# Kernel optimization log

Measured on AMD Instinct MI355X. Metric: run time of the kernel, lower is better.

The kernel has to match this reference:

```python
import jax, jax.numpy as jnp
import numpy as np

B, S, D = 2, 2048, 768          # batch, n_ctx, d_model
NQK, DQK = 12, 64               # n_qk_heads, d_qk_head
NOV, DOV = 768, 1               # n_ov_heads, d_ov_head
R = NOV // NQK                  # OV heads per QK head
VKV = 4                         # virtual_kv_num
BASE = 10000.0
SCALE = DQK ** 0.5              # cfg.attn_scale default


def _rotary_sin_cos():
    # TransformerLens-style (non-adjacent-pairs): freq repeated as (2 d)
    pos = jnp.arange(S, dtype=jnp.float32)
    freq = BASE ** (jnp.arange(0, DQK, 2, dtype=jnp.float32) / DQK)
    freq = jnp.concatenate([freq, freq])          # [DQK]
    angles = pos[:, None] / freq[None, :]         # [S, DQK]
    return jnp.sin(angles), jnp.cos(angles)


def _apply_rotary(x, sin, cos):
    # x: [b, pos, head, DQK]; rotary_dim == d_qk_head so full rotation
    half = DQK // 2
    rot = jnp.concatenate([-x[..., half:], x[..., :half]], axis=-1)
    return x * cos[None, :, None, :] + rot * sin[None, :, None, :]


def setup_inputs() -> dict:
    key = jax.random.key(0)
    ks = jax.random.split(key, 7)
    std_qk = (2.0 / (D * DQK)) ** 0.5   # kaiming fan_in (d_model*d_head)
    std_ov = (2.0 / (D * DOV)) ** 0.5
    std_o = (2.0 / (DOV * D)) ** 0.5
    sin, cos = _rotary_sin_cos()
    return {
        "resid": jax.random.normal(ks[0], (B, S, D), jnp.float32),
        "W_Q": jax.random.normal(ks[1], (NQK, D, DQK), jnp.float32) * std_qk,
        "W_K": jax.random.normal(ks[2], (NQK, D, DQK), jnp.float32) * std_qk,
        "W_V": jax.random.normal(ks[3], (NOV, D, DOV), jnp.float32) * std_ov,
        "W_O": jax.random.normal(ks[4], (NOV, DOV, D), jnp.float32) * std_o,
        "b_Q": jnp.zeros((NQK, DQK), jnp.float32),
        "b_K": jnp.zeros((NQK, DQK), jnp.float32),
        "b_V": jnp.zeros((NOV, DOV), jnp.float32),
        "virtual_k": jax.random.normal(ks[5], (VKV, NQK, DQK), jnp.float32) * (2.0 / (NQK * DQK)) ** 0.5,
        "virtual_v": jnp.zeros((VKV, NOV, DOV), jnp.float32),  # init zeros, requires_grad=False
        "rotary_sin": sin,
        "rotary_cos": cos,
    }


def reference(resid, W_Q, W_K, W_V, W_O, b_Q, b_K, b_V,
              virtual_k, virtual_v, rotary_sin, rotary_cos):
    # q/k/v projections: per-head low-rank maps + bias  -> [b, s, h, d]
    q = jnp.einsum('bsm,hmd->bshd', resid, W_Q) + b_Q
    k = jnp.einsum('bsm,hmd->bshd', resid, W_K) + b_K
    v = jnp.einsum('bsm,hmd->bshd', resid, W_V) + b_V
    # rotary on q and k
    q = _apply_rotary(q, rotary_sin, rotary_cos)
    k = _apply_rotary(k, rotary_sin, rotary_cos)
    # append virtual KV tokens at the end of the key axis
    k = jnp.concatenate([k, jnp.broadcast_to(virtual_k[None], (B, VKV, NQK, DQK))], axis=1)
    v = jnp.concatenate([v, jnp.broadcast_to(virtual_v[None], (B, VKV, NOV, DOV))], axis=1)
    # full attention scores [b, nqk, S, S+VKV]
    scores = jnp.einsum('bqhd,bkhd->bhqk', q, k) / SCALE
    # causal mask: tril(ones(S, S+VKV), diagonal=VKV) -> key j visible iff j <= i + VKV
    qi = jnp.arange(S)[:, None]
    kj = jnp.arange(S + VKV)[None, :]
    mask = kj <= qi + VKV
    scores = jnp.where(mask[None, None], scores, -jnp.inf)
    pattern = jax.nn.softmax(scores, axis=-1)
    pattern = jnp.where(jnp.isnan(pattern), 0.0, pattern)
    # group OV heads by QK head: v [b, k, NOV, DOV] -> [b, NQK, R, k, DOV]
    v_r = jnp.transpose(v, (0, 2, 1, 3)).reshape(B, NQK, R, S + VKV, DOV)
    z = jnp.einsum('bnqk,bnrkh->bnrqh', pattern, v_r)       # [b, NQK, R, S, DOV]
    z = z.reshape(B, NOV, S, DOV).transpose(0, 2, 1, 3)      # [b, S, NOV, DOV]
    out = jnp.einsum('bqhd,hdm->bqm', z, W_O)                # cal_out (no b_O)
    return out
```

## Files before the change

kernel.cpp:

```cpp
#include <hip/hip_runtime.h>

typedef __attribute__((ext_vector_type(8))) __bf16 bf16x8;
typedef __attribute__((ext_vector_type(4))) __bf16 bf16x4;
typedef __attribute__((ext_vector_type(4))) float  f32x4;

__device__ __forceinline__ void gld_lds16(const void* g, void* l) {
  __builtin_amdgcn_global_load_lds(
      (const __attribute__((address_space(1))) unsigned int*)g,
      (__attribute__((address_space(3))) unsigned int*)l, 16, 0, 0);
}


__global__ __launch_bounds__(256) void prep_kernel(
    const float* __restrict__ resid, const float* __restrict__ WQ,
    const float* __restrict__ WK, const float* __restrict__ WV,
    const float* __restrict__ WO,
    __bf16* __restrict__ Rb, __bf16* __restrict__ Wt1, __bf16* __restrict__ Wt2)
{
  int t = blockIdx.x * 256 + threadIdx.x;
  if (t < 3145728) { Rb[t] = (__bf16)resid[t]; return; }
  t -= 3145728;
  if (t < 1769472) {
    int nn = t / 768, k = t - nn * 768;
    float v;
    if (nn < 768)       v = WQ[(nn >> 6) * 49152 + k * 64 + (nn & 63)];
    else if (nn < 1536) v = WK[((nn - 768) >> 6) * 49152 + k * 64 + ((nn - 768) & 63)];
    else                v = WV[(nn - 1536) * 768 + k];
    Wt1[t] = (__bf16)v;
    return;
  }
  t -= 1769472;
  int nn = t / 768, k = t - nn * 768;
  Wt2[t] = (__bf16)WO[k * 768 + nn];
}

template<int OUTF>
__global__ __launch_bounds__(256) void gemm_bt(
    const __bf16* __restrict__ A, const __bf16* __restrict__ Bt,
    void* __restrict__ C, int M, int N, int K, int ldc)
{
  __shared__ __align__(16) char smem[32768];
  char* a_lds = smem;
  char* b_lds = smem + 16384;
  const int tid = threadIdx.x;
  const int l = tid & 63, wv = tid >> 6;
  const int wr = wv >> 1, wc = wv & 1;
  const int l15 = l & 15, lg = l >> 4;
  const int m0 = blockIdx.y * 128, n0 = blockIdx.x * 128;
  const int sw = (l15 & 7) << 4;

  f32x4 acc[4][4] = {};

  for (int k0 = 0; k0 < K; k0 += 64) {
    __syncthreads();
#pragma unroll
    for (int c = 0; c < 4; ++c) {
      int idx = c * 256 + tid;
      int row = idx >> 3, slt = idx & 7;
      gld_lds16(A + (m0 + row) * K + k0 + ((slt ^ (row & 7)) * 8), a_lds + idx * 16);
    }
#pragma unroll
    for (int c = 0; c < 4; ++c) {
      int idx = c * 256 + tid;
      int row = idx >> 3, slt = idx & 7;
      gld_lds16(Bt + (n0 + row) * K + k0 + ((slt ^ (row & 7)) * 8), b_lds + idx * 16);
    }
    __syncthreads();
#pragma unroll
    for (int kk = 0; kk < 2; ++kk) {
      bf16x8 af[4], bfr[4];
#pragma unroll
      for (int i = 0; i < 4; ++i) {
        int mr = wr * 64 + i * 16 + l15;
        af[i]  = *(const bf16x8*)(a_lds + mr * 128 + ((lg * 16 + kk * 64) ^ sw));
        int nr = wc * 64 + i * 16 + l15;
        bfr[i] = *(const bf16x8*)(b_lds + nr * 128 + ((lg * 16 + kk * 64) ^ sw));
      }
#pragma unroll
      for (int i = 0; i < 4; ++i)
#pragma unroll
        for (int j = 0; j < 4; ++j)
          acc[i][j] = __builtin_amdgcn_mfma_f32_16x16x32_bf16(af[i], bfr[j], acc[i][j], 0, 0, 0);
    }
  }
#pragma unroll
  for (int i = 0; i < 4; ++i)
#pragma unroll
    for (int j = 0; j < 4; ++j)
#pragma unroll
      for (int r = 0; r < 4; ++r) {
        int row = m0 + wr * 64 + i * 16 + lg * 4 + r;
        int col = n0 + wc * 64 + j * 16 + l15;
        if (OUTF) ((float*)C)[row * ldc + col] = acc[i][j][r];
        else      ((__bf16*)C)[row * ldc + col] = (__bf16)acc[i][j][r];
      }
}

__global__ __launch_bounds__(256) void qk_rotary(
    const __bf16* __restrict__ qkv, const float* __restrict__ bQ,
    const float* __restrict__ bK, const float* __restrict__ vk,
    const float* __restrict__ rsin, const float* __restrict__ rcos,
    __bf16* __restrict__ Qb, __bf16* __restrict__ Kb)
{
  int t = blockIdx.x * 256 + threadIdx.x;
  int d = t & 63;
  int x = t >> 6;
  int bh = x / 2112;
  int s = x - bh * 2112;
  int b = bh / 12, h = bh - b * 12;
  int kidx = (bh * 2112 + s) * 64 + d;
  if (s < 2048) {
    const __bf16* rowp = qkv + (b * 2048 + s) * 2304;
    int c0 = h * 64 + d, c1 = h * 64 + (d ^ 32);
    float sn = rsin[s * 64 + d], cs = rcos[s * 64 + d];
    float q1 = (float)rowp[c0] + bQ[c0];
    float q2 = (float)rowp[c1] + bQ[c1];
    float k1 = (float)rowp[768 + c0] + bK[c0];
    float k2 = (float)rowp[768 + c1] + bK[c1];
    float qr = (d < 32) ? -q2 : q2;
    float kr = (d < 32) ? -k2 : k2;
    Qb[(bh * 2048 + s) * 64 + d] = (__bf16)((q1 * cs + qr * sn) * 0.125f);
    Kb[kidx] = (__bf16)(k1 * cs + kr * sn);
  } else if (s < 2052) {
    Kb[kidx] = (__bf16)vk[((s - 2048) * 12 + h) * 64 + d];
  } else {
    Kb[kidx] = (__bf16)0.0f;
  }
}

__global__ __launch_bounds__(256) void v_trans(
    const __bf16* __restrict__ qkv, const float* __restrict__ bV,
    const float* __restrict__ vv, __bf16* __restrict__ Vt)
{
  __shared__ float tile[64][65];
  int st = blockIdx.x, bh = blockIdx.y;
  int b = bh / 12, h = bh - b * 12;
  int tid = threadIdx.x;
#pragma unroll
  for (int r = 0; r < 16; ++r) {
    int li = r * 256 + tid;
    int srow = li >> 6, dcol = li & 63;
    int s = st * 64 + srow;
    float val;
    if (s < 2048)      val = (float)qkv[(b * 2048 + s) * 2304 + 1536 + h * 64 + dcol] + bV[h * 64 + dcol];
    else if (s < 2052) val = vv[(s - 2048) * 768 + h * 64 + dcol];
    else               val = 0.0f;
    tile[srow][dcol] = val;
  }
  __syncthreads();
#pragma unroll
  for (int r = 0; r < 16; ++r) {
    int li = r * 256 + tid;
    int drow = li >> 6, scol = li & 63;
    Vt[(bh * 64 + drow) * 2112 + st * 64 + scol] = (__bf16)tile[scol][drow];
  }
}

__global__ __launch_bounds__(256) void attn_kernel(
    const __bf16* __restrict__ Qb, const __bf16* __restrict__ Kb,
    const __bf16* __restrict__ Vt, __bf16* __restrict__ Z)
{
  __shared__ __align__(16) char smem[24576];
  char* k_lds = smem;
  char* v_lds = smem + 8192;
  char* p_lds = smem + 16384;
  const int tid = threadIdx.x;
  const int l = tid & 63, w = tid >> 6;
  const int l15 = l & 15, lg = l >> 4;
  const int qt = blockIdx.x, bh = blockIdx.y;
  const int b = bh / 12, n = bh - b * 12;
  const int q16 = qt * 64 + w * 16;
  const int sw = (l15 & 7) << 4;
  const int qrow = w * 16 + l15;

  const __bf16* qp = Qb + (bh * 2048 + q16 + l15) * 64 + lg * 8;
  const bf16x8 qa0 = *(const bf16x8*)qp;
  const bf16x8 qa1 = *(const bf16x8*)(qp + 32);

  f32x4 o[4] = {};
  float mrun = -1e30f, lrun = 0.0f;

  const __bf16* Kbase = Kb + bh * 2112 * 64;
  const __bf16* Vbase = Vt + bh * 64 * 2112;
  const int ntiles = qt + 2;

  for (int kt = 0; kt < ntiles; ++kt) {
    const int kt0 = kt * 64;
    __syncthreads();
#pragma unroll
    for (int c = 0; c < 2; ++c) {
      int idx = c * 256 + tid;
      int row = idx >> 3, slt = idx & 7;
      gld_lds16(Kbase + (kt0 + row) * 64 + ((slt ^ (row & 7)) * 8), k_lds + idx * 16);
    }
#pragma unroll
    for (int c = 0; c < 2; ++c) {
      int idx = c * 256 + tid;
      int row = idx >> 3, slt = idx & 7;
      gld_lds16(Vbase + row * 2112 + kt0 + ((slt ^ (row & 7)) * 8), v_lds + idx * 16);
    }
    __syncthreads();

    f32x4 sfr[4];
#pragma unroll
    for (int kb = 0; kb < 4; ++kb) {
      int krow = kb * 16 + l15;
      f32x4 a = {};
      bf16x8 ka0 = *(const bf16x8*)(k_lds + krow * 128 + ((lg * 16) ^ sw));
      bf16x8 ka1 = *(const bf16x8*)(k_lds + krow * 128 + ((lg * 16 + 64) ^ sw));
      a = __builtin_amdgcn_mfma_f32_16x16x32_bf16(ka0, qa0, a, 0, 0, 0);
      a = __builtin_amdgcn_mfma_f32_16x16x32_bf16(ka1, qa1, a, 0, 0, 0);
      sfr[kb] = a;
    }
    if (kt >= qt) {
      int qlim = q16 + l15 + 4;
#pragma unroll
      for (int kb = 0; kb < 4; ++kb)
#pragma unroll
        for (int r = 0; r < 4; ++r) {
          int kg = kt0 + kb * 16 + lg * 4 + r;
          if (kg > qlim || kg >= 2052) sfr[kb][r] = -1e30f;
        }
    }
    float tmax = -1e30f;
#pragma unroll
    for (int kb = 0; kb < 4; ++kb)
#pragma unroll
      for (int r = 0; r < 4; ++r) tmax = fmaxf(tmax, sfr[kb][r]);
    tmax = fmaxf(tmax, __shfl_xor(tmax, 16));
    tmax = fmaxf(tmax, __shfl_xor(tmax, 32));
    float mnew = fmaxf(mrun, tmax);
    float fsc = __expf(mrun - mnew);
    float rsum = 0.0f;
#pragma unroll
    for (int kb = 0; kb < 4; ++kb) {
      bf16x4 pv;
#pragma unroll
      for (int r = 0; r < 4; ++r) {
        float p = __expf(sfr[kb][r] - mnew);
        rsum += p;
        pv[r] = (__bf16)p;
      }
      *(bf16x4*)(p_lds + qrow * 128 + ((kb * 32 + lg * 8) ^ sw)) = pv;
    }
    rsum += __shfl_xor(rsum, 16);
    rsum += __shfl_xor(rsum, 32);
    lrun = lrun * fsc + rsum;
    mrun = mnew;
    f32x4 fv;
#pragma unroll
    for (int r = 0; r < 4; ++r) fv[r] = __shfl(fsc, lg * 4 + r);
#pragma unroll
    for (int dv = 0; dv < 4; ++dv) o[dv] *= fv;
#pragma unroll
    for (int kblk = 0; kblk < 2; ++kblk) {
      bf16x8 pa = *(const bf16x8*)(p_lds + qrow * 128 + ((kblk * 64 + lg * 16) ^ sw));
#pragma unroll
      for (int dv = 0; dv < 4; ++dv) {
        int vrow = dv * 16 + l15;
        bf16x8 vb = *(const bf16x8*)(v_lds + vrow * 128 + ((kblk * 64 + lg * 16) ^ sw));
        o[dv] = __builtin_amdgcn_mfma_f32_16x16x32_bf16(pa, vb, o[dv], 0, 0, 0);
      }
    }
  }
  float linv = 1.0f / lrun;
  f32x4 lv;
#pragma unroll
  for (int r = 0; r < 4; ++r) lv[r] = __shfl(linv, lg * 4 + r);
  __bf16* zbase = Z + (b * 2048 + q16) * 768 + n * 64;
#pragma unroll
  for (int dv = 0; dv < 4; ++dv)
#pragma unroll
    for (int r = 0; r < 4; ++r)
      zbase[(lg * 4 + r) * 768 + dv * 16 + l15] = (__bf16)(o[dv][r] * lv[r]);
}

extern "C" void kernel_launch(void* const* d_in, const int* in_sizes, int n_in,
                              void* d_out, int out_size, void* d_ws, size_t ws_size,
                              hipStream_t stream)
{
  const float* resid = (const float*)d_in[0];
  const float* WQ   = (const float*)d_in[1];
  const float* WK   = (const float*)d_in[2];
  const float* WV   = (const float*)d_in[3];
  const float* WO   = (const float*)d_in[4];
  const float* bQ   = (const float*)d_in[5];
  const float* bK   = (const float*)d_in[6];
  const float* bV   = (const float*)d_in[7];
  const float* vk   = (const float*)d_in[8];
  const float* vv   = (const float*)d_in[9];
  const float* rsin = (const float*)d_in[10];
  const float* rcos = (const float*)d_in[11];

  char* ws = (char*)d_ws;
  __bf16* Rb  = (__bf16*)(ws);
  __bf16* Wt1 = (__bf16*)(ws + 6291456);
  __bf16* Wt2 = (__bf16*)(ws + 9830400);
  __bf16* QKV = (__bf16*)(ws + 11010048);
  __bf16* Qb  = (__bf16*)(ws + 29884416);
  __bf16* Kb  = (__bf16*)(ws + 36175872);
  __bf16* Vt  = (__bf16*)(ws + 42663936);
  __bf16* Zb  = (__bf16*)(ws + 49152000);

  prep_kernel<<<21504, 256, 0, stream>>>(resid, WQ, WK, WV, WO, Rb, Wt1, Wt2);
  gemm_bt<0><<<dim3(18, 32), 256, 0, stream>>>(Rb, Wt1, (void*)QKV, 4096, 2304, 768, 2304);
  qk_rotary<<<12672, 256, 0, stream>>>(QKV, bQ, bK, vk, rsin, rcos, Qb, Kb);
  v_trans<<<dim3(33, 24), 256, 0, stream>>>(QKV, bV, vv, Vt);
  attn_kernel<<<dim3(32, 24), 256, 0, stream>>>(Qb, Kb, Vt, Zb);
  gemm_bt<1><<<dim3(6, 32), 256, 0, stream>>>(Zb, Wt2, d_out, 4096, 768, 768, 768);
}
```

Baseline: 213.0 us.

## Double-buffer GEMM and attention loads, vectorize prep kernels, reorder attention blocks

```diff
diff --git a/kernel.cpp b/kernel.cpp
--- a/kernel.cpp
+++ b/kernel.cpp
@@ -18,8 +18,15 @@
     __bf16* __restrict__ Rb, __bf16* __restrict__ Wt1, __bf16* __restrict__ Wt2)
 {
   int t = blockIdx.x * 256 + threadIdx.x;
-  if (t < 3145728) { Rb[t] = (__bf16)resid[t]; return; }
-  t -= 3145728;
+  if (t < 786432) {
+    f32x4 v = *(const f32x4*)(resid + (size_t)t * 4);
+    bf16x4 o;
+#pragma unroll
+    for (int j = 0; j < 4; ++j) o[j] = (__bf16)v[j];
+    *(bf16x4*)(Rb + (size_t)t * 4) = o;
+    return;
+  }
+  t -= 786432;
   if (t < 1769472) {
     int nn = t / 768, k = t - nn * 768;
     float v;
@@ -39,9 +46,7 @@
     const __bf16* __restrict__ A, const __bf16* __restrict__ Bt,
     void* __restrict__ C, int M, int N, int K, int ldc)
 {
-  __shared__ __align__(16) char smem[32768];
-  char* a_lds = smem;
-  char* b_lds = smem + 16384;
+  __shared__ __align__(16) char smem[65536];
   const int tid = threadIdx.x;
   const int l = tid & 63, wv = tid >> 6;
   const int wr = wv >> 1, wc = wv & 1;
@@ -49,23 +54,31 @@
   const int m0 = blockIdx.y * 128, n0 = blockIdx.x * 128;
   const int sw = (l15 & 7) << 4;
 
+  auto stage = [&](int buf, int k0) {
+    char* a_l = smem + buf * 32768;
+    char* b_l = a_l + 16384;
+#pragma unroll
+    for (int c = 0; c < 4; ++c) {
+      int i2 = c * 256 + tid;
+      int row = i2 >> 3, slt = i2 & 7;
+      gld_lds16(A + (size_t)(m0 + row) * K + k0 + ((slt ^ (row & 7)) * 8), a_l + i2 * 16);
+    }
+#pragma unroll
+    for (int c = 0; c < 4; ++c) {
+      int i2 = c * 256 + tid;
+      int row = i2 >> 3, slt = i2 & 7;
+      gld_lds16(Bt + (size_t)(n0 + row) * K + k0 + ((slt ^ (row & 7)) * 8), b_l + i2 * 16);
+    }
+  };
+
   f32x4 acc[4][4] = {};
-
+  stage(0, 0);
+  __syncthreads();
+  int cur = 0;
   for (int k0 = 0; k0 < K; k0 += 64) {
-    __syncthreads();
-#pragma unroll
-    for (int c = 0; c < 4; ++c) {
-      int idx = c * 256 + tid;
-      int row = idx >> 3, slt = idx & 7;
-      gld_lds16(A + (m0 + row) * K + k0 + ((slt ^ (row & 7)) * 8), a_lds + idx * 16);
-    }
-#pragma unroll
-    for (int c = 0; c < 4; ++c) {
-      int idx = c * 256 + tid;
-      int row = idx >> 3, slt = idx & 7;
-      gld_lds16(Bt + (n0 + row) * K + k0 + ((slt ^ (row & 7)) * 8), b_lds + idx * 16);
-    }
-    __syncthreads();
+    if (k0 + 64 < K) stage(cur ^ 1, k0 + 64);
+    char* a_lds = smem + cur * 32768;
+    char* b_lds = a_lds + 16384;
 #pragma unroll
     for (int kk = 0; kk < 2; ++kk) {
       bf16x8 af[4], bfr[4];
@@ -82,6 +95,8 @@
         for (int j = 0; j < 4; ++j)
           acc[i][j] = __builtin_amdgcn_mfma_f32_16x16x32_bf16(af[i], bfr[j], acc[i][j], 0, 0, 0);
     }
+    __syncthreads();
+    cur ^= 1;
   }
 #pragma unroll
   for (int i = 0; i < 4; ++i)
@@ -91,8 +106,8 @@
       for (int r = 0; r < 4; ++r) {
         int row = m0 + wr * 64 + i * 16 + lg * 4 + r;
         int col = n0 + wc * 64 + j * 16 + l15;
-        if (OUTF) ((float*)C)[row * ldc + col] = acc[i][j][r];
-        else      ((__bf16*)C)[row * ldc + col] = (__bf16)acc[i][j][r];
+        if (OUTF) ((float*)C)[(size_t)row * ldc + col] = acc[i][j][r];
+        else      ((__bf16*)C)[(size_t)row * ldc + col] = (__bf16)acc[i][j][r];
       }
 }
 
@@ -103,28 +118,67 @@
     __bf16* __restrict__ Qb, __bf16* __restrict__ Kb)
 {
   int t = blockIdx.x * 256 + threadIdx.x;
-  int d = t & 63;
-  int x = t >> 6;
-  int bh = x / 2112;
-  int s = x - bh * 2112;
-  int b = bh / 12, h = bh - b * 12;
-  int kidx = (bh * 2112 + s) * 64 + d;
-  if (s < 2048) {
-    const __bf16* rowp = qkv + (b * 2048 + s) * 2304;
-    int c0 = h * 64 + d, c1 = h * 64 + (d ^ 32);
-    float sn = rsin[s * 64 + d], cs = rcos[s * 64 + d];
-    float q1 = (float)rowp[c0] + bQ[c0];
-    float q2 = (float)rowp[c1] + bQ[c1];
-    float k1 = (float)rowp[768 + c0] + bK[c0];
-    float k2 = (float)rowp[768 + c1] + bK[c1];
-    float qr = (d < 32) ? -q2 : q2;
-    float kr = (d < 32) ? -k2 : k2;
-    Qb[(bh * 2048 + s) * 64 + d] = (__bf16)((q1 * cs + qr * sn) * 0.125f);
-    Kb[kidx] = (__bf16)(k1 * cs + kr * sn);
-  } else if (s < 2052) {
-    Kb[kidx] = (__bf16)vk[((s - 2048) * 12 + h) * 64 + d];
-  } else {
-    Kb[kidx] = (__bf16)0.0f;
+  if (t < 196608) {
+    int d0 = (t & 3) * 8;
+    int x = t >> 2;
+    int bh = x >> 11, s = x & 2047;
+    int b = bh / 12, h = bh - b * 12;
+    const __bf16* rowp = qkv + ((size_t)(b * 2048 + s)) * 2304 + h * 64;
+    bf16x8 ql = *(const bf16x8*)(rowp + d0);
+    bf16x8 qu = *(const bf16x8*)(rowp + d0 + 32);
+    bf16x8 kl = *(const bf16x8*)(rowp + 768 + d0);
+    bf16x8 ku = *(const bf16x8*)(rowp + 768 + d0 + 32);
+    const float* bql = bQ + h * 64 + d0;
+    const float* bkl = bK + h * 64 + d0;
+    const float* snp = rsin + s * 64 + d0;
+    const float* csp = rcos + s * 64 + d0;
+    f32x4 bq0 = *(const f32x4*)(bql),      bq1 = *(const f32x4*)(bql + 4);
+    f32x4 bq2 = *(const f32x4*)(bql + 32), bq3 = *(const f32x4*)(bql + 36);
+    f32x4 bk0 = *(const f32x4*)(bkl),      bk1 = *(const f32x4*)(bkl + 4);
+    f32x4 bk2 = *(const f32x4*)(bkl + 32), bk3 = *(const f32x4*)(bkl + 36);
+    f32x4 sl0 = *(const f32x4*)(snp),      sl1 = *(const f32x4*)(snp + 4);
+    f32x4 su0 = *(const f32x4*)(snp + 32), su1 = *(const f32x4*)(snp + 36);
+    f32x4 cl0 = *(const f32x4*)(csp),      cl1 = *(const f32x4*)(csp + 4);
+    f32x4 cu0 = *(const f32x4*)(csp + 32), cu1 = *(const f32x4*)(csp + 36);
+    bf16x8 qlo, quo, klo, kuo;
+#pragma unroll
+    for (int j = 0; j < 8; ++j) {
+      float snl = (j < 4) ? sl0[j & 3] : sl1[j & 3];
+      float csl = (j < 4) ? cl0[j & 3] : cl1[j & 3];
+      float snu = (j < 4) ? su0[j & 3] : su1[j & 3];
+      float csu = (j < 4) ? cu0[j & 3] : cu1[j & 3];
+      float q1 = (float)ql[j] + ((j < 4) ? bq0[j & 3] : bq1[j & 3]);
+      float q2 = (float)qu[j] + ((j < 4) ? bq2[j & 3] : bq3[j & 3]);
+      float k1 = (float)kl[j] + ((j < 4) ? bk0[j & 3] : bk1[j & 3]);
+      float k2 = (float)ku[j] + ((j < 4) ? bk2[j & 3] : bk3[j & 3]);
+      qlo[j] = (__bf16)((q1 * csl - q2 * snl) * 0.125f);
+      quo[j] = (__bf16)((q2 * csu + q1 * snu) * 0.125f);
+      klo[j] = (__bf16)(k1 * csl - k2 * snl);
+      kuo[j] = (__bf16)(k2 * csu + k1 * snu);
+    }
+    __bf16* qb = Qb + ((size_t)bh * 2048 + s) * 64;
+    __bf16* kb = Kb + ((size_t)bh * 2112 + s) * 64;
+    *(bf16x8*)(qb + d0) = qlo;  *(bf16x8*)(qb + d0 + 32) = quo;
+    *(bf16x8*)(kb + d0) = klo;  *(bf16x8*)(kb + d0 + 32) = kuo;
+    return;
+  }
+  t -= 196608;
+  if (t < 12288) {
+    int d0 = (t & 7) * 8;
+    int x = t >> 3;
+    int bh = x >> 6, sp = x & 63;
+    int h = bh % 12;
+    bf16x8 o;
+    if (sp < 4) {
+      const float* vp = vk + ((size_t)sp * 12 + h) * 64 + d0;
+      f32x4 v0 = *(const f32x4*)(vp), v1 = *(const f32x4*)(vp + 4);
+#pragma unroll
+      for (int j = 0; j < 8; ++j) o[j] = (__bf16)((j < 4) ? v0[j & 3] : v1[j & 3]);
+    } else {
+#pragma unroll
+      for (int j = 0; j < 8; ++j) o[j] = (__bf16)0.0f;
+    }
+    *(bf16x8*)(Kb + ((size_t)bh * 2112 + 2048 + sp) * 64 + d0) = o;
   }
 }
 
@@ -137,22 +191,38 @@
   int b = bh / 12, h = bh - b * 12;
   int tid = threadIdx.x;
 #pragma unroll
-  for (int r = 0; r < 16; ++r) {
-    int li = r * 256 + tid;
-    int srow = li >> 6, dcol = li & 63;
+  for (int c = 0; c < 2; ++c) {
+    int chunk = c * 256 + tid;
+    int srow = chunk >> 3, d0 = (chunk & 7) * 8;
     int s = st * 64 + srow;
-    float val;
-    if (s < 2048)      val = (float)qkv[(b * 2048 + s) * 2304 + 1536 + h * 64 + dcol] + bV[h * 64 + dcol];
-    else if (s < 2052) val = vv[(s - 2048) * 768 + h * 64 + dcol];
-    else               val = 0.0f;
-    tile[srow][dcol] = val;
+    float vals[8];
+    if (s < 2048) {
+      bf16x8 v8 = *(const bf16x8*)(qkv + ((size_t)(b * 2048 + s)) * 2304 + 1536 + h * 64 + d0);
+      const float* bvp = bV + h * 64 + d0;
+      f32x4 b0 = *(const f32x4*)(bvp), b1 = *(const f32x4*)(bvp + 4);
+#pragma unroll
+      for (int j = 0; j < 8; ++j) vals[j] = (float)v8[j] + ((j < 4) ? b0[j & 3] : b1[j & 3]);
+    } else if (s < 2052) {
+      const float* vp = vv + (size_t)(s - 2048) * 768 + h * 64 + d0;
+      f32x4 v0 = *(const f32x4*)(vp), v1 = *(const f32x4*)(vp + 4);
+#pragma unroll
+      for (int j = 0; j < 8; ++j) vals[j] = (j < 4) ? v0[j & 3] : v1[j & 3];
+    } else {
+#pragma unroll
+      for (int j = 0; j < 8; ++j) vals[j] = 0.0f;
+    }
+#pragma unroll
+    for (int j = 0; j < 8; ++j) tile[srow][d0 + j] = vals[j];
   }
   __syncthreads();
 #pragma unroll
-  for (int r = 0; r < 16; ++r) {
-    int li = r * 256 + tid;
-    int drow = li >> 6, scol = li & 63;
-    Vt[(bh * 64 + drow) * 2112 + st * 64 + scol] = (__bf16)tile[scol][drow];
+  for (int c = 0; c < 2; ++c) {
+    int chunk = c * 256 + tid;
+    int drow = chunk >> 3, s0 = (chunk & 7) * 8;
+    bf16x8 o8;
+#pragma unroll
+    for (int j = 0; j < 8; ++j) o8[j] = (__bf16)tile[s0 + j][drow];
+    *(bf16x8*)(Vt + ((size_t)bh * 64 + drow) * 2112 + st * 64 + s0) = o8;
   }
 }
 
@@ -160,114 +230,128 @@
     const __bf16* __restrict__ Qb, const __bf16* __restrict__ Kb,
     const __bf16* __restrict__ Vt, __bf16* __restrict__ Z)
 {
-  __shared__ __align__(16) char smem[24576];
-  char* k_lds = smem;
-  char* v_lds = smem + 8192;
-  char* p_lds = smem + 16384;
+  __shared__ __align__(16) char smem[40960];
+  char* p_lds = smem + 32768;
   const int tid = threadIdx.x;
   const int l = tid & 63, w = tid >> 6;
   const int l15 = l & 15, lg = l >> 4;
-  const int qt = blockIdx.x, bh = blockIdx.y;
+  const int idx = blockIdx.x;
+  const int bh = idx % 24;
+  const int qt = 31 - idx / 24;
   const int b = bh / 12, n = bh - b * 12;
   const int q16 = qt * 64 + w * 16;
   const int sw = (l15 & 7) << 4;
   const int qrow = w * 16 + l15;
 
-  const __bf16* qp = Qb + (bh * 2048 + q16 + l15) * 64 + lg * 8;
+  const __bf16* Kbase = Kb + (size_t)bh * 2112 * 64;
+  const __bf16* Vbase = Vt + (size_t)bh * 64 * 2112;
+  const int ntiles = qt + 2;
+
+  auto stage = [&](int buf, int kt0) {
+    char* k_l = smem + buf * 16384;
+    char* v_l = k_l + 8192;
+#pragma unroll
+    for (int c = 0; c < 2; ++c) {
+      int i2 = c * 256 + tid;
+      int row = i2 >> 3, slt = i2 & 7;
+      gld_lds16(Kbase + (kt0 + row) * 64 + ((slt ^ (row & 7)) * 8), k_l + i2 * 16);
+    }
+#pragma unroll
+    for (int c = 0; c < 2; ++c) {
+      int i2 = c * 256 + tid;
+      int row = i2 >> 3, slt = i2 & 7;
+      gld_lds16(Vbase + row * 2112 + kt0 + ((slt ^ (row & 7)) * 8), v_l + i2 * 16);
+    }
+  };
+
+  stage(0, 0);
+
+  const __bf16* qp = Qb + ((size_t)bh * 2048 + q16 + l15) * 64 + lg * 8;
   const bf16x8 qa0 = *(const bf16x8*)qp;
   const bf16x8 qa1 = *(const bf16x8*)(qp + 32);
 
   f32x4 o[4] = {};
   float mrun = -1e30f, lrun = 0.0f;
-
-  const __bf16* Kbase = Kb + bh * 2112 * 64;
-  const __bf16* Vbase = Vt + bh * 64 * 2112;
-  const int ntiles = qt + 2;
-
+  __syncthreads();
+
+  int cur = 0;
   for (int kt = 0; kt < ntiles; ++kt) {
     const int kt0 = kt * 64;
+    if (kt + 1 < ntiles) stage(cur ^ 1, kt0 + 64);
+    char* k_lds = smem + cur * 16384;
+    char* v_lds = k_lds + 8192;
+
+    if (kt0 <= q16 + 19) {
+      f32x4 sfr[4];
+#pragma unroll
+      for (int kb = 0; kb < 4; ++kb) {
+        int krow = kb * 16 + l15;
+        f32x4 a = {};
+        bf16x8 ka0 = *(const bf16x8*)(k_lds + krow * 128 + ((lg * 16) ^ sw));
+        bf16x8 ka1 = *(const bf16x8*)(k_lds + krow * 128 + ((lg * 16 + 64) ^ sw));
+        a = __builtin_amdgcn_mfma_f32_16x16x32_bf16(ka0, qa0, a, 0, 0, 0);
+        a = __builtin_amdgcn_mfma_f32_16x16x32_bf16(ka1, qa1, a, 0, 0, 0);
+        sfr[kb] = a;
+      }
+      if (kt >= qt) {
+        int qlim = q16 + l15 + 4;
+#pragma unroll
+        for (int kb = 0; kb < 4; ++kb)
+#pragma unroll
+          for (int r = 0; r < 4; ++r) {
+            int kg = kt0 + kb * 16 + lg * 4 + r;
+            if (kg > qlim || kg >= 2052) sfr[kb][r] = -1e30f;
+          }
+      }
+      float tmax = -1e30f;
+#pragma unroll
+      for (int kb = 0; kb < 4; ++kb)
+#pragma unroll
+        for (int r = 0; r < 4; ++r) tmax = fmaxf(tmax, sfr[kb][r]);
+      tmax = fmaxf(tmax, __shfl_xor(tmax, 16));
+      tmax = fmaxf(tmax, __shfl_xor(tmax, 32));
+      float mnew = fmaxf(mrun, tmax);
+      float fsc = __expf(mrun - mnew);
+      float rsum = 0.0f;
+#pragma unroll
+      for (int kb = 0; kb < 4; ++kb) {
+        bf16x4 pv;
+#pragma unroll
+        for (int r = 0; r < 4; ++r) {
+          float p = __expf(sfr[kb][r] - mnew);
+          rsum += p;
+          pv[r] = (__bf16)p;
+        }
+        *(bf16x4*)(p_lds + qrow * 128 + ((kb * 32 + lg * 8) ^ sw)) = pv;
+      }
+      rsum += __shfl_xor(rsum, 16);
+      rsum += __shfl_xor(rsum, 32);
+      lrun = lrun * fsc + rsum;
+      mrun = mnew;
+      f32x4 fv;
+#pragma unroll
+      for (int r = 0; r < 4; ++r) fv[r] = __shfl(fsc, lg * 4 + r);
+#pragma unroll
+      for (int dv = 0; dv < 4; ++dv) o[dv] *= fv;
+#pragma unroll
+      for (int kblk = 0; kblk < 2; ++kblk) {
+        bf16x8 pa = *(const bf16x8*)(p_lds + qrow * 128 + ((kblk * 64 + lg * 16) ^ sw));
+#pragma unroll
+        for (int dv = 0; dv < 4; ++dv) {
+          int vrow = dv * 16 + l15;
+          bf16x8 vb = *(const bf16x8*)(v_lds + vrow * 128 + ((kblk * 64 + lg * 16) ^ sw));
+          o[dv] = __builtin_amdgcn_mfma_f32_16x16x32_bf16(pa, vb, o[dv], 0, 0, 0);
+        }
+      }
+    }
     __syncthreads();
-#pragma unroll
-    for (int c = 0; c < 2; ++c) {
-      int idx = c * 256 + tid;
-      int row = idx >> 3, slt = idx & 7;
-      gld_lds16(Kbase + (kt0 + row) * 64 + ((slt ^ (row & 7)) * 8), k_lds + idx * 16);
-    }
-#pragma unroll
-    for (int c = 0; c < 2; ++c) {
-      int idx = c * 256 + tid;
-      int row = idx >> 3, slt = idx & 7;
-      gld_lds16(Vbase + row * 2112 + kt0 + ((slt ^ (row & 7)) * 8), v_lds + idx * 16);
-    }
-    __syncthreads();
-
-    f32x4 sfr[4];
-#pragma unroll
-    for (int kb = 0; kb < 4; ++kb) {
-      int krow = kb * 16 + l15;
-      f32x4 a = {};
-      bf16x8 ka0 = *(const bf16x8*)(k_lds + krow * 128 + ((lg * 16) ^ sw));
-      bf16x8 ka1 = *(const bf16x8*)(k_lds + krow * 128 + ((lg * 16 + 64) ^ sw));
-      a = __builtin_amdgcn_mfma_f32_16x16x32_bf16(ka0, qa0, a, 0, 0, 0);
-      a = __builtin_amdgcn_mfma_f32_16x16x32_bf16(ka1, qa1, a, 0, 0, 0);
-      sfr[kb] = a;
-    }
-    if (kt >= qt) {
-      int qlim = q16 + l15 + 4;
-#pragma unroll
-      for (int kb = 0; kb < 4; ++kb)
-#pragma unroll
-        for (int r = 0; r < 4; ++r) {
-          int kg = kt0 + kb * 16 + lg * 4 + r;
-          if (kg > qlim || kg >= 2052) sfr[kb][r] = -1e30f;
-        }
-    }
-    float tmax = -1e30f;
-#pragma unroll
-    for (int kb = 0; kb < 4; ++kb)
-#pragma unroll
-      for (int r = 0; r < 4; ++r) tmax = fmaxf(tmax, sfr[kb][r]);
-    tmax = fmaxf(tmax, __shfl_xor(tmax, 16));
-    tmax = fmaxf(tmax, __shfl_xor(tmax, 32));
-    float mnew = fmaxf(mrun, tmax);
-    float fsc = __expf(mrun - mnew);
-    float rsum = 0.0f;
-#pragma unroll
-    for (int kb = 0; kb < 4; ++kb) {
-      bf16x4 pv;
-#pragma unroll
-      for (int r = 0; r < 4; ++r) {
-        float p = __expf(sfr[kb][r] - mnew);
-        rsum += p;
-        pv[r] = (__bf16)p;
-      }
-      *(bf16x4*)(p_lds + qrow * 128 + ((kb * 32 + lg * 8) ^ sw)) = pv;
-    }
-    rsum += __shfl_xor(rsum, 16);
-    rsum += __shfl_xor(rsum, 32);
-    lrun = lrun * fsc + rsum;
-    mrun = mnew;
-    f32x4 fv;
-#pragma unroll
-    for (int r = 0; r < 4; ++r) fv[r] = __shfl(fsc, lg * 4 + r);
-#pragma unroll
-    for (int dv = 0; dv < 4; ++dv) o[dv] *= fv;
-#pragma unroll
-    for (int kblk = 0; kblk < 2; ++kblk) {
-      bf16x8 pa = *(const bf16x8*)(p_lds + qrow * 128 + ((kblk * 64 + lg * 16) ^ sw));
-#pragma unroll
-      for (int dv = 0; dv < 4; ++dv) {
-        int vrow = dv * 16 + l15;
-        bf16x8 vb = *(const bf16x8*)(v_lds + vrow * 128 + ((kblk * 64 + lg * 16) ^ sw));
-        o[dv] = __builtin_amdgcn_mfma_f32_16x16x32_bf16(pa, vb, o[dv], 0, 0, 0);
-      }
-    }
+    cur ^= 1;
   }
   float linv = 1.0f / lrun;
   f32x4 lv;
 #pragma unroll
   for (int r = 0; r < 4; ++r) lv[r] = __shfl(linv, lg * 4 + r);
-  __bf16* zbase = Z + (b * 2048 + q16) * 768 + n * 64;
+  __bf16* zbase = Z + ((size_t)b * 2048 + q16) * 768 + n * 64;
 #pragma unroll
   for (int dv = 0; dv < 4; ++dv)
 #pragma unroll
@@ -302,10 +386,10 @@
   __bf16* Vt  = (__bf16*)(ws + 42663936);
   __bf16* Zb  = (__bf16*)(ws + 49152000);
 
-  prep_kernel<<<21504, 256, 0, stream>>>(resid, WQ, WK, WV, WO, Rb, Wt1, Wt2);
+  prep_kernel<<<12288, 256, 0, stream>>>(resid, WQ, WK, WV, WO, Rb, Wt1, Wt2);
   gemm_bt<0><<<dim3(18, 32), 256, 0, stream>>>(Rb, Wt1, (void*)QKV, 4096, 2304, 768, 2304);
-  qk_rotary<<<12672, 256, 0, stream>>>(QKV, bQ, bK, vk, rsin, rcos, Qb, Kb);
+  qk_rotary<<<816, 256, 0, stream>>>(QKV, bQ, bK, vk, rsin, rcos, Qb, Kb);
   v_trans<<<dim3(33, 24), 256, 0, stream>>>(QKV, bV, vv, Vt);
-  attn_kernel<<<dim3(32, 24), 256, 0, stream>>>(Qb, Kb, Vt, Zb);
+  attn_kernel<<<768, 256, 0, stream>>>(Qb, Kb, Vt, Zb);
   gemm_bt<1><<<dim3(6, 32), 256, 0, stream>>>(Zb, Wt2, d_out, 4096, 768, 768, 768);
 }
```

Result: faster. 189.6 us (-11.0%).
